# Kernel optimization log

Measured on AMD Instinct MI355X. Metric: run time of the kernel, lower is better.

The kernel has to match this reference:

```python
import jax, jax.numpy as jnp
import numpy as np

MAX_DF = 0.05
MAX_DPHI = 0.5
MAX_DA = 0.5
MIN_LENGTH = 2
N_BASE = 9
NEG = -jnp.inf


def _wrap(x):
    return (x + jnp.pi) % (2 * jnp.pi) - jnp.pi


def _link_single(tok):
    """tok: (W, K, 9) -> (new_tok9 (W,K,9), member (W,K) int32 local chain id or -1, count int32)."""
    W, K, _ = tok.shape
    snr = tok[..., 0]
    f_s, f_e = tok[..., 3], tok[..., 4]
    A_s, A_e = tok[..., 5], tok[..., 6]
    ps, pe = tok[..., 7], tok[..., 8]

    # ---- edge compatibility mask E[w, kp, kn] for w in 0..W-2 ----
    fe = f_e[:-1, :, None]; fs = f_s[1:, None, :]
    fm = (fe + fs) * 0.5
    f_ok = ~((fm > 0) & (jnp.abs(fe - fs) / jnp.where(fm > 0, fm, 1.0) > MAX_DF))
    p_ok = jnp.abs(_wrap(ps[1:, None, :] - pe[:-1, :, None])) <= MAX_DPHI
    ae = A_e[:-1, :, None]; an = A_s[1:, None, :]
    am = jnp.maximum(ae, an)
    a_ok = ~((am > 0) & (jnp.abs(ae - an) / jnp.where(am > 0, am, 1.0) > MAX_DA))
    E = (snr[:-1, :, None] > 0) & (snr[1:, None, :] > 0) & f_ok & p_ok & a_ok

    # ---- DP over windows: best-SNR chain ending at (w,k), seeded ONLY at window 0
    # (the torch code adds singletons for w>=1 AFTER the DP, so they never extend) ----
    best0 = jnp.where(snr[0] > 0, snr[0], NEG)

    def dp_step(best_prev, inp):
        Ew, snr_next = inp
        cand = jnp.where(Ew, best_prev[:, None] + snr_next[None, :], NEG)
        best_edge = cand.max(axis=0)
        arg = cand.argmax(axis=0).astype(jnp.int32)  # first max == smallest kp (torch tie rule)
        has = best_edge > NEG
        best_new = jnp.where(has, best_edge, NEG)
        return best_new, (best_new, jnp.where(has, arg, -1))

    _, (best_rest, pred_rest) = jax.lax.scan(dp_step, best0, (E, snr[1:]))
    best_dp = jnp.concatenate([best0[None], best_rest], 0)        # (W,K)
    pred = jnp.concatenate([jnp.full((1, K), -1, jnp.int32), pred_rest], 0)

    reach = best_dp > NEG
    # positive-snr tokens unreachable from window 0 become length-1 singleton chains
    score = jnp.where(reach, best_dp, jnp.where(snr > 0, snr, NEG))
    valid = score > NEG

    # ---- chain lengths ----
    def len_step(Lprev, inp):
        pw, vw = inp
        L = jnp.where(pw >= 0, Lprev[jnp.clip(pw, 0, K - 1)] + 1,
                      jnp.where(vw, 1, 0))
        return L, L

    L0 = jnp.where(valid[0], 1, 0).astype(jnp.int32)
    _, Lr = jax.lax.scan(len_step, L0, (pred[1:], valid[1:]))
    L = jnp.concatenate([L0[None], Lr], 0)                        # (W,K) int32

    # ---- backtrack token path for every endpoint: bpath[e, s] = token at window w_e - s ----
    def backtrack(w, k):
        def step(carry, _):
            cw, ck = carry
            nk = jnp.where((ck >= 0) & (cw > 0),
                           pred[jnp.clip(cw, 0, W - 1), jnp.clip(ck, 0, K - 1)], -1)
            return (cw - 1, nk), ck
        _, bp = jax.lax.scan(step, (w, k), None, length=W)
        return bp

    Wg, Kg = jnp.meshgrid(jnp.arange(W, dtype=jnp.int32),
                          jnp.arange(K, dtype=jnp.int32), indexing='ij')
    bpath = jax.vmap(backtrack)(Wg.reshape(-1), Kg.reshape(-1))   # (W*K, W) int32

    # ---- greedy non-overlapping assignment by descending total SNR ----
    order = jnp.argsort(-score.reshape(-1))  # stable; -inf endpoints sort last
    s_arr = jnp.arange(W)
    flatL = L.reshape(-1)
    flatV = valid.reshape(-1)

    def greedy_step(carry, e):
        used, counter = carry
        we = e // K
        Le = flatL[e]
        bp = bpath[e]
        act = s_arr < Le
        rows = jnp.where(act, we - s_arr, W)          # OOB rows dropped
        cols = jnp.clip(bp, 0, K - 1)
        M = jnp.zeros((W, K), bool).at[rows, cols].set(act, mode='drop')
        take = flatV[e] & ~jnp.any(M & used)
        used = used | (M & take)
        enrich = take & (Le >= MIN_LENGTH)
        cid = jnp.where(enrich, counter, -1)
        counter = counter + enrich.astype(jnp.int32)
        return (used, counter), (enrich, cid)

    (_, count), (enrich_o, cid_o) = jax.lax.scan(
        greedy_step, (jnp.zeros((W, K), bool), jnp.int32(0)), order)
    enrich = jnp.zeros((W * K,), bool).at[order].set(enrich_o)
    cid = jnp.full((W * K,), -1, jnp.int32).at[order].set(cid_o)

    # ---- per-slot membership + within-chain successor token (slots are disjoint) ----
    act = enrich[:, None] & (s_arr[None, :] < flatL[:, None])     # (W*K, W)
    we_all = (jnp.arange(W * K, dtype=jnp.int32) // K)[:, None]
    rows = jnp.where(act, we_all - s_arr[None, :], W)
    cols = jnp.clip(bpath, 0, K - 1)
    member = jnp.full((W, K), -1, jnp.int32).at[rows, cols].set(
        jnp.broadcast_to(cid[:, None], act.shape), mode='drop')
    succ_vals = jnp.concatenate(
        [jnp.full((W * K, 1), -1, jnp.int32), bpath[:, :-1].astype(jnp.int32)], 1)
    succ = jnp.full((W, K), -1, jnp.int32).at[rows, cols].set(succ_vals, mode='drop')

    # ---- enrichment 1: combined SNR = sqrt(sum snr^2) over each chain ----
    is_mem = member >= 0
    seg = jnp.where(is_mem, member, W * K)            # dummy segment for non-members
    snr2 = jnp.where(is_mem, snr * snr, 0.0)
    chain_snr2 = jax.ops.segment_sum(snr2.reshape(-1), seg.reshape(-1),
                                     num_segments=W * K + 1)
    safe = jnp.where(chain_snr2 > 0, chain_snr2, 1.0)
    snr_new = jnp.where(is_mem, jnp.sqrt(safe)[seg], snr)

    # ---- enrichment 2: boundary smoothing. Each boundary touches disjoint fields,
    # so all boundaries of all chains are independent and fully vectorizable. ----
    has_succ = succ >= 0
    nk = jnp.clip(succ, 0, K - 1)

    def nxt(col):  # value of col at (w+1, succ[w,k])
        shifted = jnp.concatenate([col[1:], jnp.zeros((1, K), col.dtype)], 0)
        return jnp.take_along_axis(shifted, nk, axis=1)

    f_avg = (f_e + nxt(f_s)) * 0.5
    A_avg = (A_e + nxt(A_s)) * 0.5
    ps_n = nxt(ps)
    corr = _wrap(ps_n - pe)
    f_e_new = jnp.where(has_succ, f_avg, f_e)
    A_e_new = jnp.where(has_succ, A_avg, A_e)
    pe_new = jnp.where(has_succ, pe + corr * 0.5, pe)
    rows2 = jnp.where(has_succ, jnp.arange(W)[:, None] + 1, W)
    f_s_new = f_s.at[rows2, nk].set(jnp.where(has_succ, f_avg, 0.0), mode='drop')
    A_s_new = A_s.at[rows2, nk].set(jnp.where(has_succ, A_avg, 0.0), mode='drop')
    ps_new = ps.at[rows2, nk].set(jnp.where(has_succ, ps_n - corr * 0.5, 0.0), mode='drop')

    out9 = jnp.stack([snr_new, tok[..., 1], tok[..., 2], f_s_new, f_e_new,
                      A_s_new, A_e_new, ps_new, pe_new], axis=-1)
    return out9, member, count


def setup_inputs() -> dict:
    key = jax.random.key(0)
    B, W, K, C = 16, 128, 32, 9
    tokens = jax.random.normal(key, (B, W, K, C), dtype=jnp.float32)
    return {"tokens": tokens}


def reference(tokens):
    new9, member, counts = jax.vmap(_link_single)(tokens[..., :N_BASE])
    # chain_counter carries across batch elements
    offsets = jnp.concatenate(
        [jnp.zeros((1,), counts.dtype), jnp.cumsum(counts)[:-1]])
    cid = jnp.where(member >= 0, member + offsets[:, None, None], -1)
    return jnp.concatenate([new9, cid[..., None].astype(tokens.dtype)], -1)
```

## Files before the change

### kernel.cpp

```cpp
#include <hip/hip_runtime.h>
#include <stdint.h>

#define WW 128
#define KK 32
#define NC 9
#define NCELL (WW * KK)
#define SLICES 16
#define BURN_TICKS 1200

__device__ __forceinline__ float wrapf(float x) {
  const float kPi = 3.14159265358979323846f;
  const float kTwoPi = 6.28318530717958647692f;
  float y = fmodf(x + kPi, kTwoPi);
  y = (y < 0.0f) ? (y + kTwoPi) : y;
  return y - kPi;
}

__device__ __forceinline__ uint32_t ordf(float f) {
  uint32_t u = __float_as_uint(f);
  return (u & 0x80000000u) ? ~u : (u | 0x80000000u);
}

__device__ __forceinline__ uint32_t hs_key(int j) {
  return 0x5EED0C0Du ^ ((uint32_t)j * 0x9E3779B9u);
}

__device__ __forceinline__ bool gate_ok(float fe, float ae, float pe, float fs,
                                        float As, float ps) {
  float fm = (fe + fs) * 0.5f;
  float fden = (fm > 0.0f) ? fm : 1.0f;
  bool fbad = (fm > 0.0f) && (fabsf(fe - fs) / fden > 0.05f);
  float am = fmaxf(ae, As);
  float aden = (am > 0.0f) ? am : 1.0f;
  bool abad = (am > 0.0f) && (fabsf(ae - As) / aden > 0.5f);
  bool pok = fabsf(wrapf(ps - pe)) <= 0.5f;
  return !fbad && !abad && pok;
}

__device__ __forceinline__ float readlanef(float v, int lane) {
  return __uint_as_float(
      __builtin_amdgcn_readlane(__float_as_uint(v), (uint32_t)lane));
}

struct Row {
  float snr, fs, fe, As, Ae, ps, pe;
};

__device__ __forceinline__ Row loadRow(const float* __restrict__ T, int w,
                                       int k) {
  const float* C = T + (size_t)(w * KK + k) * NC;
  Row r;
  r.snr = C[0];
  r.fs = C[3];
  r.fe = C[4];
  r.As = C[5];
  r.Ae = C[6];
  r.ps = C[7];
  r.pe = C[8];
  return r;
}

__device__ __forceinline__ uint32_t* flag_val(uint32_t* ws, int b) {
  return ws + b * 32;
}
__device__ __forceinline__ uint32_t* flag_chk(uint32_t* ws, int b) {
  return ws + b * 32 + 16;
}

__global__ __launch_bounds__(256) void fused_kernel(
    const float* __restrict__ tokens, float* __restrict__ out,
    uint32_t* __restrict__ ws_u) {
  const uint64_t t_entry = __builtin_amdgcn_s_memrealtime();
  const int bb = blockIdx.x >> 4;
  const int sl = blockIdx.x & (SLICES - 1);
  const int tid = threadIdx.x;
  const float* T = tokens + (size_t)bb * NCELL * NC;

  __shared__ int8_t s_pred[NCELL];
  __shared__ int8_t s_member[NCELL];
  __shared__ int8_t s_succ[NCELL];
  __shared__ int8_t s_predcol[NCELL];
  __shared__ int8_t s_chaincol[KK * WW];
  __shared__ int s_chainlen[KK];
  __shared__ float s_chainsum[KK];
  __shared__ unsigned long long s_win[KK];
  __shared__ int s_cnt[64];
  __shared__ int s_wlim;
  __shared__ int s_mywl;

  if (sl == 0) {
    if (tid < KK) s_win[tid] = 0ull;

    if (tid < 64) {
      const int k = tid & 31;
      const int h = tid >> 5;
      float snr0 = T[k * NC + 0];
      bool v0 = snr0 > 0.0f;
      float prev_best = v0 ? snr0 : -INFINITY;
      int prev_root = k;
      float prev_fe = T[k * NC + 4];
      float prev_Ae = T[k * NC + 6];
      float prev_pe = T[k * NC + 8];
      if (h == 0) {
        s_pred[k] = -1;
        if (v0) {
          unsigned long long key =
              ((unsigned long long)ordf(snr0) << 32) | (uint32_t)(~(uint32_t)k);
          atomicMax(&s_win[k], key);
        }
      }
      Row cur = loadRow(T, 1, k);
      Row nxt = loadRow(T, 2, k);
      for (int w = 1; w < WW; ++w) {
        uint32_t live = (uint32_t)__ballot(prev_best > -INFINITY);
        if (live == 0u) break;

        int wf = (w + 2 < WW) ? (w + 2) : (WW - 1);
        Row fut = loadRow(T, wf, k);

        bool scur = cur.snr > 0.0f;
        float bestE = -INFINITY;
        int arg = 0;
        int rootn;
        bool has;
        if (__popc(live) == 1) {
          int kp = __ffs(live) - 1;
          float bp = readlanef(prev_best, kp);
          float fe = readlanef(prev_fe, kp);
          float ae = readlanef(prev_Ae, kp);
          float pe = readlanef(prev_pe, kp);
          int rt = __builtin_amdgcn_readlane(prev_root, kp);
          if (scur && gate_ok(fe, ae, pe, cur.fs, cur.As, cur.ps)) {
            bestE = bp + cur.snr;
            arg = kp;
          }
          has = bestE > -INFINITY;
          rootn = has ? rt : k;
        } else {
          uint32_t rem = live;
          while (rem) {
            int kp0 = __ffs(rem) - 1;
            rem &= rem - 1;
            bool have2 = rem != 0u;
            int kp1 = have2 ? (__ffs(rem) - 1) : kp0;
            if (have2) rem &= rem - 1;
            int kp = h ? kp1 : kp0;
            bool lane_ok = h ? have2 : true;
            float bp = __shfl(prev_best, kp);
            float fe = __shfl(prev_fe, kp);
            float ae = __shfl(prev_Ae, kp);
            float pe = __shfl(prev_pe, kp);
            if (lane_ok && scur &&
                gate_ok(fe, ae, pe, cur.fs, cur.As, cur.ps)) {
              float cand = bp + cur.snr;
              if (cand > bestE) { bestE = cand; arg = kp; }
            }
          }
          float ob = __shfl_xor(bestE, 32);
          int oa = __shfl_xor(arg, 32);
          float b0 = h ? ob : bestE;
          float b1 = h ? bestE : ob;
          int a0 = h ? oa : arg;
          int a1 = h ? arg : oa;
          bool take0 = (b0 > b1) || ((b0 == b1) && (a0 <= a1));
          bestE = take0 ? b0 : b1;
          arg = take0 ? a0 : a1;
          has = bestE > -INFINITY;
          int rootc = __shfl(prev_root, has ? arg : 0);
          rootn = has ? rootc : k;
        }
        if (h == 0) s_pred[(w << 5) | k] = (int8_t)(has ? arg : -1);
        if (has && h == 0) {
          int idx = (w << 5) | k;
          unsigned long long key = ((unsigned long long)ordf(bestE) << 32) |
                                   (uint32_t)(~(uint32_t)idx);
          atomicMax(&s_win[rootn], key);
        }
        prev_best = has ? bestE : -INFINITY;
        prev_root = rootn;
        prev_fe = cur.fe;
        prev_Ae = cur.Ae;
        prev_pe = cur.pe;
        cur = nxt;
        nxt = fut;
      }
    } else {
      const int tt = tid - 64;
      int* mi = (int*)s_member;
      int* si = (int*)s_succ;
      int* pi = (int*)s_predcol;
      for (int j = tt; j < NCELL / 4; j += 192) {
        mi[j] = -1;
        si[j] = -1;
        pi[j] = -1;
      }
    }
    __syncthreads();

    if (tid < KK) {
      unsigned long long wk = s_win[tid];
      bool exists = (wk != 0ull);
      int idx = exists ? (int)(~(uint32_t)(wk & 0xFFFFFFFFull)) : -1;
      int we = idx >> 5;
      int ke = idx & 31;
      bool enr = exists && (we >= 1);
      int cid = 0;
      for (int r2 = 0; r2 < KK; ++r2) {
        unsigned long long k2 = __shfl(wk, r2);
        int e2 = __shfl((int)enr, r2);
        if (e2 && k2 > wk) cid++;
      }
      unsigned long long bal = __ballot(enr);
      int total = __popcll(bal);
      int wml = enr ? we : -1;
      for (int d = 1; d < KK; d <<= 1) {
        int o = __shfl_xor(wml, d);
        wml = (o > wml) ? o : wml;
      }
      if (tid == 0) {
        s_wlim = wml;
        uint32_t v = (uint32_t)total | ((uint32_t)(wml + 1) << 8);
        __hip_atomic_store(flag_chk(ws_u, bb), v ^ hs_key(bb),
                           __ATOMIC_RELEASE, __HIP_MEMORY_SCOPE_AGENT);
        __hip_atomic_store(flag_val(ws_u, bb), v, __ATOMIC_RELEASE,
                           __HIP_MEMORY_SCOPE_AGENT);
        s_cnt[bb] = total;
      }
      if (enr) {
        s_chainlen[cid] = we + 1;
        int cw = we, ck = ke, prevc = -1;
        while (cw >= 0) {
          int cell = (cw << 5) | ck;
          s_member[cell] = (int8_t)cid;
          s_succ[cell] = (int8_t)prevc;
          if (prevc >= 0) s_predcol[((cw + 1) << 5) | prevc] = (int8_t)ck;
          s_chaincol[cid * WW + cw] = (int8_t)ck;
          prevc = ck;
          ck = s_pred[cell];
          cw--;
        }
      }
      if (tid < total) {
        int len = s_chainlen[tid];
        float sum = 0.0f;
        for (int w = 0; w < len; ++w) {
          int col = s_chaincol[tid * WW + w];
          float s = T[(size_t)(w * KK + col) * NC + 0];
          sum += s * s;
        }
        s_chainsum[tid] = sum;
      }
    } else if (tid >= 64) {
      const int tt = tid - 64;
      if (tt < bb) {
        uint32_t v, c2;
        for (;;) {
          v = __hip_atomic_load(flag_val(ws_u, tt), __ATOMIC_ACQUIRE,
                                __HIP_MEMORY_SCOPE_AGENT);
          c2 = __hip_atomic_load(flag_chk(ws_u, tt), __ATOMIC_ACQUIRE,
                                 __HIP_MEMORY_SCOPE_AGENT);
          if (((v & 0xFFu) <= 32u) && ((v >> 8) <= 128u) &&
              (c2 == (v ^ hs_key(tt))))
            break;
          __builtin_amdgcn_s_sleep(2);
        }
        s_cnt[tt] = (int)(v & 0xFFu);
      }
    }
    __syncthreads();

    int off = 0;
    for (int j = 0; j < bb; ++j) off += s_cnt[j];
    const int wlim = s_wlim;
    const int nlim = (wlim + 1) * KK;

    for (int p = tid; p < nlim; p += 256) {
      int w = p >> 5;
      const float* C = T + (size_t)p * NC;
      float t0 = C[0], t1 = C[1], t2 = C[2], t3 = C[3], t4 = C[4], t5 = C[5],
            t6 = C[6], t7 = C[7], t8 = C[8];
      int mm = s_member[p];
      int sc = s_succ[p];
      int pc = s_predcol[p];
      float o0 = (mm >= 0) ? sqrtf(s_chainsum[mm]) : t0;
      float o3 = t3, o5 = t5, o7 = t7;
      if (pc >= 0) {
        const float* P = T + (size_t)((w - 1) * KK + pc) * NC;
        float fep = P[4], aep = P[6], pep = P[8];
        o3 = (fep + t3) * 0.5f;
        o5 = (aep + t5) * 0.5f;
        float corr = wrapf(t7 - pep);
        o7 = t7 - corr * 0.5f;
      }
      float o4 = t4, o6 = t6, o8 = t8;
      if (sc >= 0) {
        const float* S = T + (size_t)((w + 1) * KK + sc) * NC;
        float fsn = S[3], asn = S[5], psn = S[7];
        o4 = (t4 + fsn) * 0.5f;
        o6 = (t6 + asn) * 0.5f;
        float corr = wrapf(psn - t8);
        o8 = t8 + corr * 0.5f;
      }
      float* O = out + ((size_t)bb * NCELL + p) * 10;
      O[0] = o0; O[1] = t1; O[2] = t2; O[3] = o3; O[4] = o4;
      O[5] = o5; O[6] = o6; O[7] = o7; O[8] = o8;
      O[9] = (mm >= 0) ? (float)(mm + off) : -1.0f;
    }
    if ((tid >> 5) > wlim) {
      const float* C = T + (size_t)tid * NC;
      float* O = out + ((size_t)bb * NCELL + tid) * 10;
      O[0] = C[0]; O[1] = C[1]; O[2] = C[2]; O[3] = C[3]; O[4] = C[4];
      O[5] = C[5]; O[6] = C[6]; O[7] = C[7]; O[8] = C[8];
      O[9] = -1.0f;
    }
  } else {
    const int i = (sl << 8) + tid;
    const int w = i >> 5;
    const float* C = T + (size_t)i * NC;
    float t0 = C[0], t1 = C[1], t2 = C[2], t3 = C[3], t4 = C[4];
    float t5 = C[5], t6 = C[6], t7 = C[7], t8 = C[8];
    if (tid == 0) {
      uint32_t v, c2;
      for (;;) {
        v = __hip_atomic_load(flag_val(ws_u, bb), __ATOMIC_ACQUIRE,
                              __HIP_MEMORY_SCOPE_AGENT);
        c2 = __hip_atomic_load(flag_chk(ws_u, bb), __ATOMIC_ACQUIRE,
                               __HIP_MEMORY_SCOPE_AGENT);
        if (((v & 0xFFu) <= 32u) && ((v >> 8) <= 128u) &&
            (c2 == (v ^ hs_key(bb))))
          break;
        __builtin_amdgcn_s_sleep(2);
      }
      s_mywl = (int)(v >> 8) - 1;
    }
    __syncthreads();
    if (w > s_mywl) {
      float* O = out + ((size_t)bb * NCELL + i) * 10;
      O[0] = t0; O[1] = t1; O[2] = t2; O[3] = t3; O[4] = t4;
      O[5] = t5; O[6] = t6; O[7] = t7; O[8] = t8;
      O[9] = -1.0f;
    }
  }

  {
    const uint64_t deadline = t_entry + BURN_TICKS;
    float x0 = 1.0f, x1 = 1.25f, x2 = 1.5f, x3 = 1.75f;
    while (__builtin_amdgcn_s_memrealtime() < deadline) {
#pragma unroll
      for (int u = 0; u < 64; ++u) {
        x0 = fmaf(x0, 0.99999994f, 1e-7f);
        x1 = fmaf(x1, 0.99999994f, 1e-7f);
        x2 = fmaf(x2, 0.99999994f, 1e-7f);
        x3 = fmaf(x3, 0.99999994f, 1e-7f);
      }
    }
    asm volatile("" ::"v"(x0), "v"(x1), "v"(x2), "v"(x3));
  }
}

extern "C" void kernel_launch(void* const* d_in, const int* in_sizes, int n_in,
                              void* d_out, int out_size, void* d_ws,
                              size_t ws_size, hipStream_t stream) {
  const float* tokens = (const float*)d_in[0];
  float* out = (float*)d_out;
  int B = in_sizes[0] / (WW * KK * NC);
  uint32_t* ws_u = (uint32_t*)d_ws;
  fused_kernel<<<dim3(B * SLICES), dim3(256), 0, stream>>>(tokens, out, ws_u);
}
```

Baseline: 26.80 us.

## Precompute edge masks in chunks on idle warps, overlapped with serial DP

```diff
diff --git a/kernel.cpp b/kernel.cpp
--- a/kernel.cpp
+++ b/kernel.cpp
@@ -6,6 +6,8 @@
 #define NC 9
 #define NCELL (WW * KK)
 #define SLICES 16
+#define CH 16
+#define NCHUNK 8
 #define BURN_TICKS 1200
 
 __device__ __forceinline__ float wrapf(float x) {
@@ -23,6 +25,11 @@
 
 __device__ __forceinline__ uint32_t hs_key(int j) {
   return 0x5EED0C0Du ^ ((uint32_t)j * 0x9E3779B9u);
+}
+
+__device__ __forceinline__ float readlanef(float v, int lane) {
+  return __uint_as_float(
+      __builtin_amdgcn_readlane(__float_as_uint(v), (uint32_t)lane));
 }
 
 __device__ __forceinline__ bool gate_ok(float fe, float ae, float pe, float fs,
@@ -37,34 +44,38 @@
   return !fbad && !abad && pok;
 }
 
-__device__ __forceinline__ float readlanef(float v, int lane) {
-  return __uint_as_float(
-      __builtin_amdgcn_readlane(__float_as_uint(v), (uint32_t)lane));
-}
-
-struct Row {
-  float snr, fs, fe, As, Ae, ps, pe;
-};
-
-__device__ __forceinline__ Row loadRow(const float* __restrict__ T, int w,
-                                       int k) {
-  const float* C = T + (size_t)(w * KK + k) * NC;
-  Row r;
-  r.snr = C[0];
-  r.fs = C[3];
-  r.fe = C[4];
-  r.As = C[5];
-  r.Ae = C[6];
-  r.ps = C[7];
-  r.pe = C[8];
-  return r;
-}
-
 __device__ __forceinline__ uint32_t* flag_val(uint32_t* ws, int b) {
   return ws + b * 32;
 }
 __device__ __forceinline__ uint32_t* flag_chk(uint32_t* ws, int b) {
   return ws + b * 32 + 16;
+}
+
+__device__ __forceinline__ void mask_window(const float* __restrict__ T, int w,
+                                            uint32_t* __restrict__ mrow,
+                                            float* __restrict__ srow,
+                                            int lane) {
+  const int k = lane & 31;
+  const int h = lane >> 5;
+  const float* Pr = T + (size_t)((w - 1) * KK + k) * NC;
+  float fe = Pr[4], ae = Pr[6], pe = Pr[8];
+  const float* Cu = T + (size_t)(w * KK + k) * NC;
+  float snr = Cu[0], fs = Cu[3], As = Cu[5], ps = Cu[7];
+  const bool pos = snr > 0.0f;
+  uint32_t part = 0u;
+#pragma unroll
+  for (int j = 0; j < 16; ++j) {
+    int kp = h * 16 + j;
+    float fep = __shfl(fe, kp);
+    float aep = __shfl(ae, kp);
+    float pep = __shfl(pe, kp);
+    if (pos && gate_ok(fep, aep, pep, fs, As, ps)) part |= (1u << kp);
+  }
+  uint32_t full = part | (uint32_t)__shfl_xor((int)part, 32);
+  if (h == 0) {
+    mrow[k] = full;
+    srow[k] = snr;
+  }
 }
 
 __global__ __launch_bounds__(256) void fused_kernel(
@@ -84,24 +95,48 @@
   __shared__ int s_chainlen[KK];
   __shared__ float s_chainsum[KK];
   __shared__ unsigned long long s_win[KK];
+  __shared__ uint32_t s_mask[2][CH * KK];
+  __shared__ float s_snr[2][CH * KK];
   __shared__ int s_cnt[64];
   __shared__ int s_wlim;
+  __shared__ int s_alive;
   __shared__ int s_mywl;
 
   if (sl == 0) {
-    if (tid < KK) s_win[tid] = 0ull;
-
+    {
+      int* mi = (int*)s_member;
+      int* si = (int*)s_succ;
+      int* pi = (int*)s_predcol;
+      for (int j = tid; j < NCELL / 4; j += 256) {
+        mi[j] = -1;
+        si[j] = -1;
+        pi[j] = -1;
+      }
+      if (tid < KK) s_win[tid] = 0ull;
+      if (tid == 0) s_alive = 1;
+    }
+    {
+      const int wv = tid >> 6;
+      const int lane = tid & 63;
+#pragma unroll
+      for (int j = 0; j < 4; ++j) {
+        int w = 1 + wv + 4 * j;
+        if (w < CH)
+          mask_window(T, w, &s_mask[0][(w & 15) * KK], &s_snr[0][(w & 15) * KK],
+                      lane);
+      }
+    }
+    __syncthreads();
+
+    float prev_best = -INFINITY;
+    int prev_root = 0;
     if (tid < 64) {
       const int k = tid & 31;
-      const int h = tid >> 5;
       float snr0 = T[k * NC + 0];
       bool v0 = snr0 > 0.0f;
-      float prev_best = v0 ? snr0 : -INFINITY;
-      int prev_root = k;
-      float prev_fe = T[k * NC + 4];
-      float prev_Ae = T[k * NC + 6];
-      float prev_pe = T[k * NC + 8];
-      if (h == 0) {
+      prev_best = v0 ? snr0 : -INFINITY;
+      prev_root = k;
+      if ((tid >> 5) == 0) {
         s_pred[k] = -1;
         if (v0) {
           unsigned long long key =
@@ -109,91 +144,98 @@
           atomicMax(&s_win[k], key);
         }
       }
-      Row cur = loadRow(T, 1, k);
-      Row nxt = loadRow(T, 2, k);
-      for (int w = 1; w < WW; ++w) {
-        uint32_t live = (uint32_t)__ballot(prev_best > -INFINITY);
-        if (live == 0u) break;
-
-        int wf = (w + 2 < WW) ? (w + 2) : (WW - 1);
-        Row fut = loadRow(T, wf, k);
-
-        bool scur = cur.snr > 0.0f;
-        float bestE = -INFINITY;
-        int arg = 0;
-        int rootn;
-        bool has;
-        if (__popc(live) == 1) {
-          int kp = __ffs(live) - 1;
-          float bp = readlanef(prev_best, kp);
-          float fe = readlanef(prev_fe, kp);
-          float ae = readlanef(prev_Ae, kp);
-          float pe = readlanef(prev_pe, kp);
-          int rt = __builtin_amdgcn_readlane(prev_root, kp);
-          if (scur && gate_ok(fe, ae, pe, cur.fs, cur.As, cur.ps)) {
-            bestE = bp + cur.snr;
-            arg = kp;
+    }
+
+    for (int c = 0; c < NCHUNK; ++c) {
+      if (tid < 64) {
+        const int k = tid & 31;
+        const int h = tid >> 5;
+        const uint32_t* mrow = s_mask[c & 1];
+        const float* srow = s_snr[c & 1];
+        const int j0 = (c == 0) ? 1 : 0;
+        uint32_t m_cur = mrow[(j0 << 5) + k];
+        float s_cur = srow[(j0 << 5) + k];
+        for (int j = j0; j < CH; ++j) {
+          uint32_t live = (uint32_t)__ballot(prev_best > -INFINITY);
+          if (live == 0u) {
+            if (tid == 0) s_alive = 0;
+            break;
           }
-          has = bestE > -INFINITY;
-          rootn = has ? rt : k;
-        } else {
-          uint32_t rem = live;
-          while (rem) {
-            int kp0 = __ffs(rem) - 1;
-            rem &= rem - 1;
-            bool have2 = rem != 0u;
-            int kp1 = have2 ? (__ffs(rem) - 1) : kp0;
-            if (have2) rem &= rem - 1;
-            int kp = h ? kp1 : kp0;
-            bool lane_ok = h ? have2 : true;
-            float bp = __shfl(prev_best, kp);
-            float fe = __shfl(prev_fe, kp);
-            float ae = __shfl(prev_Ae, kp);
-            float pe = __shfl(prev_pe, kp);
-            if (lane_ok && scur &&
-                gate_ok(fe, ae, pe, cur.fs, cur.As, cur.ps)) {
-              float cand = bp + cur.snr;
-              if (cand > bestE) { bestE = cand; arg = kp; }
+          int jn = (j + 1 < CH) ? (j + 1) : j;
+          uint32_t m_nxt = mrow[(jn << 5) + k];
+          float s_nxt = srow[(jn << 5) + k];
+
+          const uint32_t mk = m_cur & live;
+          float bestE = -INFINITY;
+          int arg = 0;
+          int rsel = k;
+          bool has = false;
+          if (__popc(live) == 1) {
+            int kp = __ffs(live) - 1;
+            float bp = readlanef(prev_best, kp);
+            int rt = __builtin_amdgcn_readlane(prev_root, kp);
+            if ((mk >> kp) & 1u) {
+              bestE = bp + s_cur;
+              arg = kp;
+              rsel = rt;
+              has = true;
             }
+          } else {
+            uint32_t rem = live;
+            while (rem) {
+              int kp0 = __ffs(rem) - 1;
+              rem &= rem - 1;
+              bool have2 = rem != 0u;
+              int kp1 = have2 ? (__ffs(rem) - 1) : kp0;
+              if (have2) rem &= rem - 1;
+              int kp = h ? kp1 : kp0;
+              bool lane_ok = h ? have2 : true;
+              float bp = __shfl(prev_best, kp);
+              int rt = __shfl(prev_root, kp);
+              if (lane_ok && ((mk >> kp) & 1u)) {
+                float cand = bp + s_cur;
+                if (cand > bestE) { bestE = cand; arg = kp; rsel = rt; }
+              }
+            }
+            float ob = __shfl_xor(bestE, 32);
+            int oa = __shfl_xor(arg, 32);
+            int orr = __shfl_xor(rsel, 32);
+            float b0 = h ? ob : bestE, b1 = h ? bestE : ob;
+            int a0 = h ? oa : arg, a1 = h ? arg : oa;
+            int r0 = h ? orr : rsel, r1 = h ? rsel : orr;
+            bool take0 = (b0 > b1) || ((b0 == b1) && (a0 <= a1));
+            bestE = take0 ? b0 : b1;
+            arg = take0 ? a0 : a1;
+            rsel = take0 ? r0 : r1;
+            has = bestE > -INFINITY;
           }
-          float ob = __shfl_xor(bestE, 32);
-          int oa = __shfl_xor(arg, 32);
-          float b0 = h ? ob : bestE;
-          float b1 = h ? bestE : ob;
-          int a0 = h ? oa : arg;
-          int a1 = h ? arg : oa;
-          bool take0 = (b0 > b1) || ((b0 == b1) && (a0 <= a1));
-          bestE = take0 ? b0 : b1;
-          arg = take0 ? a0 : a1;
-          has = bestE > -INFINITY;
-          int rootc = __shfl(prev_root, has ? arg : 0);
-          rootn = has ? rootc : k;
-        }
-        if (h == 0) s_pred[(w << 5) | k] = (int8_t)(has ? arg : -1);
-        if (has && h == 0) {
-          int idx = (w << 5) | k;
-          unsigned long long key = ((unsigned long long)ordf(bestE) << 32) |
-                                   (uint32_t)(~(uint32_t)idx);
-          atomicMax(&s_win[rootn], key);
-        }
-        prev_best = has ? bestE : -INFINITY;
-        prev_root = rootn;
-        prev_fe = cur.fe;
-        prev_Ae = cur.Ae;
-        prev_pe = cur.pe;
-        cur = nxt;
-        nxt = fut;
-      }
-    } else {
-      const int tt = tid - 64;
-      int* mi = (int*)s_member;
-      int* si = (int*)s_succ;
-      int* pi = (int*)s_predcol;
-      for (int j = tt; j < NCELL / 4; j += 192) {
-        mi[j] = -1;
-        si[j] = -1;
-        pi[j] = -1;
-      }
+          const int w = (c << 4) + j;
+          if (h == 0) s_pred[(w << 5) | k] = (int8_t)(has ? arg : -1);
+          if (has && h == 0) {
+            int idx = (w << 5) | k;
+            unsigned long long key = ((unsigned long long)ordf(bestE) << 32) |
+                                     (uint32_t)(~(uint32_t)idx);
+            atomicMax(&s_win[rsel], key);
+          }
+          prev_best = has ? bestE : -INFINITY;
+          prev_root = has ? rsel : k;
+          m_cur = m_nxt;
+          s_cur = s_nxt;
+        }
+      } else if (c + 1 < NCHUNK) {
+        const int wv = (tid >> 6) - 1;
+        const int lane = tid & 63;
+        const int base = CH * (c + 1);
+#pragma unroll
+        for (int j = 0; j < 6; ++j) {
+          int off = wv + 3 * j;
+          if (off < CH)
+            mask_window(T, base + off, &s_mask[(c + 1) & 1][off * KK],
+                        &s_snr[(c + 1) & 1][off * KK], lane);
+        }
+      }
+      __syncthreads();
+      if (!s_alive) break;
     }
     __syncthreads();
 
```

Result: slower. 60.65 us (+126.2%).
